# Kernel tuning notes

Hardware: AMD Instinct MI355X
Metric: run time of the kernel (lower is better)

## Reference

```python
import jax, jax.numpy as jnp
import numpy as np

N = 8192      # atoms
E = 4096      # edges (become transformer tokens)
E2 = 65536    # edges of second graph y
VOCAB = 119
DE = 200      # node_features == embedding_dim
D = 256
H = 8
L = 2
DFF = 2048


def _bn(x, g, b, eps=1e-6):
    m = x.mean(0)
    v = x.var(0)
    return (x - m) * jax.lax.rsqrt(v + eps) * g + b


def _ln(x, g, b, eps=1e-5):
    m = x.mean(-1, keepdims=True)
    v = ((x - m) ** 2).mean(-1, keepdims=True)
    return (x - m) * jax.lax.rsqrt(v + eps) * g + b


def _gcn(x, ei, W, b):
    # PyG GCNConv: add self loops, symmetric deg^-1/2 normalization
    n = x.shape[0]
    loop = jnp.arange(n)
    src = jnp.concatenate([ei[0], loop])
    dst = jnp.concatenate([ei[1], loop])
    deg = jax.ops.segment_sum(jnp.ones(src.shape[0], x.dtype), dst, num_segments=n)
    dinv = jnp.where(deg > 0, jax.lax.rsqrt(jnp.maximum(deg, 1e-12)), 0.0)
    msg = (x @ W)[src] * (dinv[src] * dinv[dst])[:, None]
    return jax.ops.segment_sum(msg, dst, num_segments=n) + b


def _mha(x, wi, bi, wo, bo):
    S, d = x.shape
    dh = d // H
    q, k, v = jnp.split(x @ wi + bi, 3, axis=1)
    q = q.reshape(S, H, dh)
    k = k.reshape(S, H, dh)
    v = v.reshape(S, H, dh)
    sc = jnp.einsum('qhd,khd->hqk', q, k) * (1.0 / np.sqrt(dh))
    a = jax.nn.softmax(sc, axis=-1)
    o = jnp.einsum('hqk,khd->qhd', a, v).reshape(S, d)
    return o @ wo + bo


def setup_inputs() -> dict:
    key = jax.random.key(0)
    ks = iter(jax.random.split(key, 64))
    nrm = lambda shape, s=0.05: jax.random.normal(next(ks), shape, jnp.float32) * s
    d = {}
    d['x'] = jax.random.randint(next(ks), (N,), 0, VOCAB)
    d['edge_index'] = jax.random.randint(next(ks), (2, E), 1, N + 1)  # 1-based, code subtracts 1
    d['pos'] = jax.random.normal(next(ks), (N, 3), jnp.float32)
    d['y'] = jax.random.randint(next(ks), (2, E2), 0, E)
    d['emb'] = nrm((VOCAB, DE), 1.0)
    d['fc1_w'] = nrm((1, DE))
    d['fc1_b'] = jnp.zeros((DE,), jnp.float32)
    d['bn4_g'] = jnp.ones((DE,), jnp.float32)
    d['bn4_b'] = jnp.zeros((DE,), jnp.float32)
    d['conv1_w'] = nrm((DE, D))
    d['conv1_b'] = jnp.zeros((D,), jnp.float32)
    d['conv2_w'] = nrm((D, D))
    d['conv2_b'] = jnp.zeros((D,), jnp.float32)
    for i in (1, 2, 3):
        d['bn%d_g' % i] = jnp.ones((D,), jnp.float32)
        d['bn%d_b' % i] = jnp.zeros((D,), jnp.float32)
    d['in_proj_w'] = nrm((L, D, 3 * D))
    d['in_proj_b'] = jnp.zeros((L, 3 * D), jnp.float32)
    d['out_proj_w'] = nrm((L, D, D))
    d['out_proj_b'] = jnp.zeros((L, D), jnp.float32)
    d['ln1_g'] = jnp.ones((L, D), jnp.float32)
    d['ln1_b'] = jnp.zeros((L, D), jnp.float32)
    d['ln2_g'] = jnp.ones((L, D), jnp.float32)
    d['ln2_b'] = jnp.zeros((L, D), jnp.float32)
    d['ff1_w'] = nrm((L, D, DFF))
    d['ff1_b'] = jnp.zeros((L, DFF), jnp.float32)
    d['ff2_w'] = nrm((L, DFF, D))
    d['ff2_b'] = jnp.zeros((L, D), jnp.float32)
    d['fc3_w'] = nrm((D, 1))
    d['fc3_b'] = jnp.zeros((1,), jnp.float32)
    d['fc4_w'] = nrm((D, 9))
    d['fc4_b'] = jnp.zeros((9,), jnp.float32)
    return d


def reference(x, edge_index, pos, y, emb, fc1_w, fc1_b, bn4_g, bn4_b,
              conv1_w, conv1_b, conv2_w, conv2_b,
              bn1_g, bn1_b, bn2_g, bn2_b, bn3_g, bn3_b,
              in_proj_w, in_proj_b, out_proj_w, out_proj_b,
              ln1_g, ln1_b, ln2_g, ln2_b, ff1_w, ff1_b, ff2_w, ff2_b,
              fc3_w, fc3_b, fc4_w, fc4_b):
    h = emb[x]                                   # [N, DE]
    ei = edge_index - 1
    row, col = ei[0], ei[1]
    ef = jnp.linalg.norm(pos[col] - pos[row], axis=1, keepdims=True)  # [E,1]
    ef = _bn(ef @ fc1_w + fc1_b, bn4_g, bn4_b)   # [E, DE]
    h = h[row] + h[col] + ef                     # [E, DE] edges -> tokens
    h = jax.nn.leaky_relu(_gcn(h, y, conv1_w, conv1_b))
    h = _bn(h, bn1_g, bn1_b)
    h = jax.nn.leaky_relu(h + _gcn(h, y, conv2_w, conv2_b))
    h = _bn(h, bn2_g, bn2_b)
    # post-norm TransformerEncoder (unbatched seq of length E), dropout=0
    for i in range(L):
        h = _ln(h + _mha(h, in_proj_w[i], in_proj_b[i], out_proj_w[i], out_proj_b[i]),
                ln1_g[i], ln1_b[i])
        ff = jax.nn.relu(h @ ff1_w[i] + ff1_b[i]) @ ff2_w[i] + ff2_b[i]
        h = _ln(h + ff, ln2_g[i], ln2_b[i])
    h = jax.nn.leaky_relu(h)
    h = _bn(h, bn3_g, bn3_b)
    sym_out = h @ fc3_w + fc3_b
    asym_out = h @ fc4_w + fc4_b
    return (sym_out, asym_out)
```

## Files before the change

### kernel.cpp

```cpp
#include <hip/hip_runtime.h>
#include <math.h>

#define ETOK 4096
#define NE2  65536
#define DEF  200
#define DM   256
#define NH   8
#define DH   32
#define DFFN 2048
#define NKS  4

#define QSCALE_LOG2E 0.25503474f

typedef __attribute__((ext_vector_type(8))) short bfrag8;
typedef __attribute__((ext_vector_type(4))) float f32x4;
typedef __attribute__((ext_vector_type(4))) short short4v;

__device__ __forceinline__ unsigned short f2bf(float f) {
  union { float f; unsigned u; } v; v.f = f;
  unsigned u = v.u + 0x7fffu + ((v.u >> 16) & 1u);
  return (unsigned short)(u >> 16);
}
__device__ __forceinline__ unsigned cvt_pk_bf16(float lo, float hi) {
  unsigned r;
  asm("v_cvt_pk_bf16_f32 %0, %1, %2" : "=v"(r) : "v"(lo), "v"(hi));
  return r;
}

__device__ __forceinline__ float wave_sum(float v) {
#pragma unroll
  for (int off = 32; off > 0; off >>= 1) v += __shfl_xor(v, off);
  return v;
}
__device__ __forceinline__ float block_sum(float v, float* red) {
  v = wave_sum(v);
  int lane = threadIdx.x & 63, w = threadIdx.x >> 6;
  if (lane == 0) red[w] = v;
  __syncthreads();
  float t = red[0] + red[1] + red[2] + red[3];
  __syncthreads();
  return t;
}

__global__ void edge_dist_kernel(const int* __restrict__ ei, const float* __restrict__ pos,
                                 float* __restrict__ ef0, float* __restrict__ stats) {
  __shared__ float red[4];
  int e = blockIdx.x * 256 + threadIdx.x;
  int r = ei[e] - 1;
  int c = ei[ETOK + e] - 1;
  float dx = pos[c * 3 + 0] - pos[r * 3 + 0];
  float dy = pos[c * 3 + 1] - pos[r * 3 + 1];
  float dz = pos[c * 3 + 2] - pos[r * 3 + 2];
  float d = sqrtf(dx * dx + dy * dy + dz * dz);
  ef0[e] = d;
  float s = block_sum(d, red);
  float s2 = block_sum(d * d, red);
  if (threadIdx.x == 0) {
    atomicAdd(stats + 0, s);
    atomicAdd(stats + 1, s2);
  }
}

__global__ void token_build_kernel(const int* __restrict__ x, const int* __restrict__ ei,
                                   const float* __restrict__ emb, const float* __restrict__ fc1_w,
                                   const float* __restrict__ bn4_g, const float* __restrict__ bn4_b,
                                   const float* __restrict__ ef0, const float* __restrict__ stats,
                                   unsigned short* __restrict__ tokbf) {
  int e = blockIdx.x;
  int j = threadIdx.x;
  float m = stats[0] * (1.0f / 4096.0f);
  float v = stats[1] * (1.0f / 4096.0f) - m * m;
  int xr = x[ei[e] - 1];
  int xc = x[ei[ETOK + e] - 1];
  float dd = ef0[e] - m;
  float val = 0.f;
  if (j < DEF) {
    float w = fc1_w[j];
    float s = w * rsqrtf(v * w * w + 1e-6f) * bn4_g[j];
    val = emb[(size_t)xr * DEF + j] + emb[(size_t)xc * DEF + j] + dd * s + bn4_b[j];
  }
  tokbf[(size_t)e * 256 + j] = f2bf(val);
}

__global__ void deg_count_kernel(const int* __restrict__ y, int* __restrict__ deg) {
  int e = blockIdx.x * 256 + threadIdx.x;
  atomicAdd(&deg[y[NE2 + e]], 1);
}
__global__ void dinv_kernel(const int* __restrict__ deg, float* __restrict__ dinv) {
  int i = blockIdx.x * 256 + threadIdx.x;
  dinv[i] = rsqrtf((float)(deg[i] + 1));
}
__global__ void scan_kernel(const int* __restrict__ deg, int* __restrict__ off,
                            int* __restrict__ cursor) {
  __shared__ int part[256];
  int t = threadIdx.x;
  int v[16];
  int s = 0;
#pragma unroll
  for (int i = 0; i < 16; ++i) {
    v[i] = deg[t * 16 + i];
    s += v[i];
  }
  part[t] = s;
  __syncthreads();
  if (t == 0) {
    int a = 0;
#pragma unroll 1
    for (int i = 0; i < 256; ++i) {
      int tmp = part[i];
      part[i] = a;
      a += tmp;
    }
    off[4096] = a;
  }
  __syncthreads();
  int a = part[t];
#pragma unroll
  for (int i = 0; i < 16; ++i) {
    off[t * 16 + i] = a;
    cursor[t * 16 + i] = a;
    a += v[i];
  }
}
__global__ void fill_kernel(const int* __restrict__ y, int* __restrict__ cursor,
                            int* __restrict__ srcl) {
  int e = blockIdx.x * 256 + threadIdx.x;
  int s = y[e];
  int d = y[NE2 + e];
  int slot = atomicAdd(&cursor[d], 1);
  srcl[slot] = s;
}

template <int RES, int ACT>
__global__ __launch_bounds__(256) void gather_kernel(const float* __restrict__ xw,
                                                     const int* __restrict__ off,
                                                     const int* __restrict__ srcl,
                                                     const float* __restrict__ dinv,
                                                     const float* __restrict__ bias,
                                                     const float* __restrict__ resid,
                                                     float* __restrict__ out) {
  __shared__ int slds[256];
  __shared__ float dlds[256];
  const int d = blockIdx.x;
  const int c = threadIdx.x;
  const int b0 = off[d], b1 = off[d + 1];
  const float dd = dinv[d];
  float acc = 0.f;
  for (int base = b0; base < b1; base += 256) {
    int n = min(256, b1 - base);
    __syncthreads();
    if (c < n) {
      int s = srcl[base + c];
      slds[c] = s;
      dlds[c] = dinv[s];
    }
    __syncthreads();
    for (int j = 0; j < n; ++j) {
      int s = slds[j];
      acc = fmaf(xw[(size_t)s * DM + c], dlds[j], acc);
    }
  }
  size_t idx = (size_t)d * DM + c;
  float v = bias[c] + xw[idx] * dd * dd + acc * dd;
  if (RES) v += resid[idx];
  if (ACT) v = v > 0.f ? v : 0.01f * v;
  out[idx] = v;
}

struct WEntry {
  const float* src;
  unsigned short* dst;
  int K, N, KP, tilesN, ntiles;
};
struct WPack {
  WEntry e[10];
};
__global__ __launch_bounds__(256) void wtrans_all_kernel(WPack p) {
  __shared__ float tl[32][33];
  int t = blockIdx.x;
  int i = 0;
  while (t >= p.e[i].ntiles) {
    t -= p.e[i].ntiles;
    ++i;
  }
  const WEntry w = p.e[i];
  int nb = (t % w.tilesN) * 32;
  int kb = (t / w.tilesN) * 32;
  int tx = threadIdx.x & 31, ty = threadIdx.x >> 5;
#pragma unroll
  for (int r = ty; r < 32; r += 8) {
    int k = kb + r, n = nb + tx;
    tl[r][tx] = (k < w.K && n < w.N) ? w.src[(size_t)k * w.N + n] : 0.f;
  }
  __syncthreads();
#pragma unroll
  for (int r = ty; r < 32; r += 8) {
    int n = nb + r, k = kb + tx;
    if (n < w.N) w.dst[(size_t)n * w.KP + k] = f2bf(tl[tx][r]);
  }
}

template <int BM, int BN, int OUTBF, int ACT, int QS>
__global__ __launch_bounds__(256) void mfma_gemm(const unsigned short* __restrict__ A,
                                                 const unsigned short* __restrict__ Bt,
                                                 const float* __restrict__ bias,
                                                 void* __restrict__ Cout, int M, int N, int K) {
  constexpr int BK = 64;
  constexpr int TM = BM / 32, TN = BN / 32;
  constexpr int ACH = BM / 32, BCH = BN / 32;
  __shared__ unsigned short Alds[BM * BK];
  __shared__ unsigned short Blds[BN * BK];
  const int tid = threadIdx.x;
  const int lane = tid & 63, wid = tid >> 6;
  const int g = lane >> 4, q = lane & 15;
  const int wr = wid >> 1, wc = wid & 1;
  const int m0 = blockIdx.y * BM, n0 = blockIdx.x * BN;

  f32x4 acc[TM][TN];
#pragma unroll
  for (int i = 0; i < TM; ++i)
#pragma unroll
    for (int j = 0; j < TN; ++j) acc[i][j] = (f32x4){0.f, 0.f, 0.f, 0.f};

  for (int k0 = 0; k0 < K; k0 += BK) {
    __syncthreads();
#pragma unroll
    for (int c = 0; c < ACH; ++c) {
      int chunk = wid * ACH + c;
      int row = chunk * 8 + (lane >> 3);
      int cb = ((lane & 7) * 16) ^ ((row & 7) << 4);
      const char* gp = (const char*)A + ((size_t)(m0 + row) * K + k0) * 2 + cb;
      __builtin_amdgcn_global_load_lds(
          (const __attribute__((address_space(1))) unsigned int*)gp,
          (__attribute__((address_space(3))) unsigned int*)(Alds + chunk * 512), 16, 0, 0);
    }
#pragma unroll
    for (int c = 0; c < BCH; ++c) {
      int chunk = wid * BCH + c;
      int row = chunk * 8 + (lane >> 3);
      int cb = ((lane & 7) * 16) ^ ((row & 7) << 4);
      const char* gp = (const char*)Bt + ((size_t)(n0 + row) * K + k0) * 2 + cb;
      __builtin_amdgcn_global_load_lds(
          (const __attribute__((address_space(1))) unsigned int*)gp,
          (__attribute__((address_space(3))) unsigned int*)(Blds + chunk * 512), 16, 0, 0);
    }
    __syncthreads();
#pragma unroll
    for (int ks = 0; ks < 2; ++ks) {
      bfrag8 af[TM], bfr[TN];
#pragma unroll
      for (int mi = 0; mi < TM; ++mi) {
        int row = wr * (BM / 2) + mi * 16 + q;
        int cb = (ks * 64 + g * 16) ^ ((row & 7) << 4);
        af[mi] = *(const bfrag8*)((const char*)Alds + row * 128 + cb);
      }
#pragma unroll
      for (int ni = 0; ni < TN; ++ni) {
        int row = wc * (BN / 2) + ni * 16 + q;
        int cb = (ks * 64 + g * 16) ^ ((row & 7) << 4);
        bfr[ni] = *(const bfrag8*)((const char*)Blds + row * 128 + cb);
      }
#pragma unroll
      for (int mi = 0; mi < TM; ++mi)
#pragma unroll
        for (int ni = 0; ni < TN; ++ni)
          acc[mi][ni] = __builtin_amdgcn_mfma_f32_16x16x32_bf16(af[mi], bfr[ni], acc[mi][ni], 0, 0, 0);
    }
  }
#pragma unroll
  for (int mi = 0; mi < TM; ++mi) {
    int row = m0 + wr * (BM / 2) + mi * 16 + g * 4;
#pragma unroll
    for (int ni = 0; ni < TN; ++ni) {
      int col = n0 + wc * (BN / 2) + ni * 16 + q;
      float bv = bias ? bias[col] : 0.f;
#pragma unroll
      for (int r = 0; r < 4; ++r) {
        float v = acc[mi][ni][r] + bv;
        if (QS && col < DM) v *= QSCALE_LOG2E;
        if (ACT == 1) v = fmaxf(v, 0.f);
        if (OUTBF)
          ((unsigned short*)Cout)[(size_t)(row + r) * N + col] = f2bf(v);
        else
          ((float*)Cout)[(size_t)(row + r) * N + col] = v;
      }
    }
  }
}

template <int LEAKY>
__global__ void col_stats_kernel(const float* __restrict__ x, int C, float* __restrict__ mean,
                                 float* __restrict__ var) {
  __shared__ float red[4];
  int c = blockIdx.x;
  float s = 0.f, s2 = 0.f;
  for (int r = threadIdx.x; r < ETOK; r += 256) {
    float v = x[(size_t)r * C + c];
    if (LEAKY) v = v > 0.f ? v : 0.01f * v;
    s += v;
    s2 += v * v;
  }
  float ts = block_sum(s, red);
  float ts2 = block_sum(s2, red);
  if (threadIdx.x == 0) {
    float m = ts * (1.0f / 4096.0f);
    mean[c] = m;
    var[c] = ts2 * (1.0f / 4096.0f) - m * m;
  }
}
template <int LEAKY>
__global__ void bn_apply_kernel(const float* __restrict__ x, const float* __restrict__ mean,
                                const float* __restrict__ var, const float* __restrict__ g,
                                const float* __restrict__ b, float* __restrict__ outf,
                                unsigned short* __restrict__ outb, int C) {
  size_t i = (size_t)blockIdx.x * 256 + threadIdx.x;
  int c = (int)(i % C);
  float v0 = x[i];
  if (LEAKY) v0 = v0 > 0.f ? v0 : 0.01f * v0;
  float v = (v0 - mean[c]) * rsqrtf(var[c] + 1e-6f) * g[c] + b[c];
  outf[i] = v;
  if (outb) outb[i] = f2bf(v);
}

__global__ __launch_bounds__(256) void attn_mfma_kernel(const unsigned short* __restrict__ qkv,
                                                        float* __restrict__ Opart,
                                                        float* __restrict__ MLpart) {
  const int h = blockIdx.y;
  const int qblk = blockIdx.x * 64;
  const int chunk = blockIdx.z;
  const int tid = threadIdx.x;
  const int wid = tid >> 6, lane = tid & 63;
  const int g = lane >> 4, q = lane & 15;

  __shared__ unsigned short Klds[64][40];
  __shared__ unsigned int Vtw[32][32];
  __shared__ unsigned short Plds[4][16][72];

  bfrag8 qfrag;
  {
    const unsigned short* qp = qkv + (size_t)(qblk + wid * 16 + q) * 768 + h * DH + g * 8;
    qfrag = *(const bfrag8*)qp;
  }
  const f32x4 zero = {0.f, 0.f, 0.f, 0.f};

  float m = -1e30f, lsum = 0.f;
  f32x4 o0 = zero, o1 = zero;

  const int kbeg = chunk * (ETOK / NKS);
  const int kend = kbeg + (ETOK / NKS);
  for (int kt = kbeg; kt < kend; kt += 64) {
    __syncthreads();
    {
      int key = tid >> 2, db = (tid & 3) * 8;
      const unsigned short* kp = qkv + (size_t)(kt + key) * 768 + DM + h * DH + db;
      *(bfrag8*)&Klds[key][db] = *(const bfrag8*)kp;

      int kp2 = tid >> 3, dc = (tid & 7) * 4;
      const unsigned short* v0 = qkv + (size_t)(kt + kp2 * 2) * 768 + 2 * DM + h * DH + dc;
      const unsigned short* v1 = v0 + 768;
      short4v a = *(const short4v*)v0;
      short4v bq = *(const short4v*)v1;
#pragma unroll
      for (int j = 0; j < 4; ++j) {
        int d = dc + j;
        unsigned pk = (unsigned)(unsigned short)a[j] | ((unsigned)(unsigned short)bq[j] << 16);
        Vtw[d][kp2 ^ (((d >> 3) & 3) << 3)] = pk;
      }
    }
    __syncthreads();

    f32x4 st[4];
    __builtin_amdgcn_s_setprio(1);
#pragma unroll
    for (int t = 0; t < 4; ++t) {
      bfrag8 kf = *(const bfrag8*)&Klds[t * 16 + q][g * 8];
      st[t] = __builtin_amdgcn_mfma_f32_16x16x32_bf16(kf, qfrag, zero, 0, 0, 0);
    }
    __builtin_amdgcn_s_setprio(0);

    float tmax = fmaxf(fmaxf(st[0][0], st[0][1]), fmaxf(st[0][2], st[0][3]));
#pragma unroll
    for (int t = 1; t < 4; ++t)
      tmax = fmaxf(tmax, fmaxf(fmaxf(st[t][0], st[t][1]), fmaxf(st[t][2], st[t][3])));
    tmax = fmaxf(tmax, __shfl_xor(tmax, 16));
    tmax = fmaxf(tmax, __shfl_xor(tmax, 32));
    if (!__all(tmax <= m + 8.0f)) {
      float mnew = fmaxf(m, tmax);
      float coef = __builtin_exp2f(m - mnew);
      lsum *= coef;
#pragma unroll
      for (int r = 0; r < 4; ++r) {
        float cr = __shfl(coef, g * 4 + r);
        o0[r] *= cr;
        o1[r] *= cr;
      }
      m = mnew;
    }

    float ps = 0.f;
    unsigned pk8[8];
#pragma unroll
    for (int t = 0; t < 4; ++t) {
      float p0 = __builtin_exp2f(st[t][0] - m);
      float p1 = __builtin_exp2f(st[t][1] - m);
      float p2 = __builtin_exp2f(st[t][2] - m);
      float p3 = __builtin_exp2f(st[t][3] - m);
      ps += (p0 + p1) + (p2 + p3);
      pk8[t * 2 + 0] = cvt_pk_bf16(p0, p1);
      pk8[t * 2 + 1] = cvt_pk_bf16(p2, p3);
    }
    lsum += ps;

#pragma unroll
    for (int t = 0; t < 4; ++t) {
      uint2 w2;
      w2.x = pk8[t * 2 + 0];
      w2.y = pk8[t * 2 + 1];
      *(uint2*)&Plds[wid][q][t * 16 + g * 4] = w2;
    }

    __builtin_amdgcn_s_setprio(1);
#pragma unroll
    for (int kg = 0; kg < 2; ++kg) {
      bfrag8 pa = *(const bfrag8*)&Plds[wid][q][kg * 32 + g * 8];
      int i0 = (kg * 16 + g * 4) ^ ((q >> 3) << 3);
      int i1 = (kg * 16 + g * 4) ^ (((2 + (q >> 3)) & 3) << 3);
      bfrag8 vb0 = *(const bfrag8*)&Vtw[q][i0];
      bfrag8 vb1 = *(const bfrag8*)&Vtw[16 + q][i1];
      o0 = __builtin_amdgcn_mfma_f32_16x16x32_bf16(pa, vb0, o0, 0, 0, 0);
      o1 = __builtin_amdgcn_mfma_f32_16x16x32_bf16(pa, vb1, o1, 0, 0, 0);
    }
    __builtin_amdgcn_s_setprio(0);
  }

  lsum += __shfl_xor(lsum, 16);
  lsum += __shfl_xor(lsum, 32);
#pragma unroll
  for (int r = 0; r < 4; ++r) {
    int row = qblk + wid * 16 + g * 4 + r;
    float* op = Opart + ((size_t)chunk * ETOK + row) * DM + h * DH;
    op[q] = o0[r];
    op[16 + q] = o1[r];
  }
  if (lane < 16) {
    int row = qblk + wid * 16 + lane;
    float* ml = MLpart + ((size_t)chunk * ETOK + row) * (NH * 2) + h * 2;
    ml[0] = m;
    ml[1] = lsum;
  }
}

__global__ __launch_bounds__(256) void attn_combine_kernel(const float* __restrict__ Opart,
                                                           const float* __restrict__ MLpart,
                                                           unsigned short* __restrict__ out) {
  __shared__ float mls[NKS][NH][2];
  const int row = blockIdx.x;
  const int c = threadIdx.x;
  if (c < NKS * NH * 2) {
    int ch = c >> 4, rem = c & 15;
    mls[ch][rem >> 1][rem & 1] = MLpart[((size_t)ch * ETOK + row) * (NH * 2) + rem];
  }
  __syncthreads();
  const int h = c >> 5;
  float mstar = mls[0][h][0];
#pragma unroll
  for (int ch = 1; ch < NKS; ++ch) mstar = fmaxf(mstar, mls[ch][h][0]);
  float lstar = 0.f, acc = 0.f;
#pragma unroll
  for (int ch = 0; ch < NKS; ++ch) {
    float w = __builtin_exp2f(mls[ch][h][0] - mstar);
    lstar = fmaf(mls[ch][h][1], w, lstar);
    acc = fmaf(Opart[((size_t)ch * ETOK + row) * DM + c], w, acc);
  }
  out[(size_t)row * DM + c] = f2bf(acc / lstar);
}

__global__ void add_ln_kernel(const float* __restrict__ x, const float* __restrict__ r,
                              float* __restrict__ outf, unsigned short* __restrict__ outb,
                              const float* __restrict__ g, const float* __restrict__ b) {
  __shared__ float red[4];
  int row = blockIdx.x, t = threadIdx.x;
  size_t idx = (size_t)row * DM + t;
  float v = x[idx] + r[idx];
  float mean = block_sum(v, red) * (1.0f / 256.0f);
  float dv = v - mean;
  float var = block_sum(dv * dv, red) * (1.0f / 256.0f);
  float o = dv * rsqrtf(var + 1e-5f) * g[t] + b[t];
  outf[idx] = o;
  outb[idx] = f2bf(o);
}

__global__ void head_kernel(const float* __restrict__ h, const float* __restrict__ fc3w,
                            const float* __restrict__ fc3b, const float* __restrict__ fc4w,
                            const float* __restrict__ fc4b, float* __restrict__ out) {
  int wave = threadIdx.x >> 6, lane = threadIdx.x & 63;
  int tok = blockIdx.x * 4 + wave;
  const float* hr = h + (size_t)tok * DM;
  float hv[4];
#pragma unroll
  for (int i = 0; i < 4; ++i) hv[i] = hr[lane * 4 + i];
  float acc = 0.f;
#pragma unroll
  for (int i = 0; i < 4; ++i) acc += hv[i] * fc3w[lane * 4 + i];
  acc = wave_sum(acc);
  if (lane == 0) out[tok] = acc + fc3b[0];
#pragma unroll
  for (int j = 0; j < 9; ++j) {
    float a = 0.f;
#pragma unroll
    for (int i = 0; i < 4; ++i) a += hv[i] * fc4w[(lane * 4 + i) * 9 + j];
    a = wave_sum(a);
    if (lane == 0) out[ETOK + (size_t)tok * 9 + j] = a + fc4b[j];
  }
}

extern "C" void kernel_launch(void* const* d_in, const int* in_sizes, int n_in,
                              void* d_out, int out_size, void* d_ws, size_t ws_size,
                              hipStream_t stream) {
  const int* x = (const int*)d_in[0];
  const int* edge_index = (const int*)d_in[1];
  const float* pos = (const float*)d_in[2];
  const int* y = (const int*)d_in[3];
  const float* emb = (const float*)d_in[4];
  const float* fc1_w = (const float*)d_in[5];
  const float* bn4_g = (const float*)d_in[7];
  const float* bn4_b = (const float*)d_in[8];
  const float* conv1_w = (const float*)d_in[9];
  const float* conv1_b = (const float*)d_in[10];
  const float* conv2_w = (const float*)d_in[11];
  const float* conv2_b = (const float*)d_in[12];
  const float* bn1_g = (const float*)d_in[13];
  const float* bn1_b = (const float*)d_in[14];
  const float* bn2_g = (const float*)d_in[15];
  const float* bn2_b = (const float*)d_in[16];
  const float* bn3_g = (const float*)d_in[17];
  const float* bn3_b = (const float*)d_in[18];
  const float* ipw = (const float*)d_in[19];
  const float* ipb = (const float*)d_in[20];
  const float* opw = (const float*)d_in[21];
  const float* opb = (const float*)d_in[22];
  const float* ln1_g = (const float*)d_in[23];
  const float* ln1_b = (const float*)d_in[24];
  const float* ln2_g = (const float*)d_in[25];
  const float* ln2_b = (const float*)d_in[26];
  const float* ff1w = (const float*)d_in[27];
  const float* ff1b = (const float*)d_in[28];
  const float* ff2w = (const float*)d_in[29];
  const float* ff2b = (const float*)d_in[30];
  const float* fc3w = (const float*)d_in[31];
  const float* fc3b = (const float*)d_in[32];
  const float* fc4w = (const float*)d_in[33];
  const float* fc4b = (const float*)d_in[34];
  float* outp = (float*)d_out;

  char* wsp = (char*)d_ws;
  auto alloc = [&](size_t bytes) {
    void* p = (void*)wsp;
    wsp += (bytes + 255) & ~(size_t)255;
    return p;
  };
  unsigned short* big_bf = (unsigned short*)alloc((size_t)ETOK * DFFN * 2);
  unsigned short* attno = (unsigned short*)alloc((size_t)ETOK * DM * 2);
  unsigned short* h_bf = (unsigned short*)alloc((size_t)ETOK * DM * 2);
  unsigned short* tok_bf = (unsigned short*)alloc((size_t)ETOK * 256 * 2);
  float* hf = (float*)alloc((size_t)ETOK * DM * 4);
  float* t1 = (float*)alloc((size_t)ETOK * DM * 4);
  float* t2 = (float*)alloc((size_t)ETOK * DM * 4);
  float* Opart = (float*)alloc((size_t)NKS * ETOK * DM * 4);
  float* MLpart = (float*)alloc((size_t)NKS * ETOK * NH * 2 * 4);
  unsigned short* c1wt = (unsigned short*)alloc(256 * 256 * 2);
  unsigned short* c2wt = (unsigned short*)alloc(256 * 256 * 2);
  unsigned short* ipwt = (unsigned short*)alloc((size_t)2 * 768 * 256 * 2);
  unsigned short* opwt = (unsigned short*)alloc((size_t)2 * 256 * 256 * 2);
  unsigned short* f1wt = (unsigned short*)alloc((size_t)2 * 2048 * 256 * 2);
  unsigned short* f2wt = (unsigned short*)alloc((size_t)2 * 256 * 2048 * 2);
  float* ef0 = (float*)alloc(ETOK * 4);
  float* dinv = (float*)alloc(ETOK * 4);
  int* deg = (int*)alloc(ETOK * 4);
  int* off = (int*)alloc((ETOK + 1) * 4);
  int* cursor = (int*)alloc(ETOK * 4);
  int* srcl = (int*)alloc(NE2 * 4);
  float* stats = (float*)alloc(8 * 4);
  float* colm = (float*)alloc(DM * 4);
  float* colv = (float*)alloc(DM * 4);

  hipMemsetAsync(stats, 0, 2 * sizeof(float), stream);
  hipMemsetAsync(deg, 0, ETOK * sizeof(int), stream);

  WPack wp;
  int ntot = 0;
  auto went = [&](int i, const float* src, unsigned short* dst, int K, int N, int KP) {
    wp.e[i].src = src;
    wp.e[i].dst = dst;
    wp.e[i].K = K;
    wp.e[i].N = N;
    wp.e[i].KP = KP;
    wp.e[i].tilesN = (N + 31) / 32;
    wp.e[i].ntiles = ((N + 31) / 32) * (KP / 32);
    ntot += wp.e[i].ntiles;
  };
  went(0, conv1_w, c1wt, 200, 256, 256);
  went(1, conv2_w, c2wt, 256, 256, 256);
  went(2, ipw, ipwt, 256, 768, 256);
  went(3, ipw + (size_t)256 * 768, ipwt + (size_t)768 * 256, 256, 768, 256);
  went(4, opw, opwt, 256, 256, 256);
  went(5, opw + (size_t)256 * 256, opwt + (size_t)256 * 256, 256, 256, 256);
  went(6, ff1w, f1wt, 256, 2048, 256);
  went(7, ff1w + (size_t)256 * 2048, f1wt + (size_t)2048 * 256, 256, 2048, 256);
  went(8, ff2w, f2wt, 2048, 256, 2048);
  went(9, ff2w + (size_t)2048 * 256, f2wt + (size_t)256 * 2048, 2048, 256, 2048);
  wtrans_all_kernel<<<ntot, 256, 0, stream>>>(wp);

  edge_dist_kernel<<<16, 256, 0, stream>>>(edge_index, pos, ef0, stats);
  deg_count_kernel<<<NE2 / 256, 256, 0, stream>>>(y, deg);
  scan_kernel<<<1, 256, 0, stream>>>(deg, off, cursor);
  dinv_kernel<<<ETOK / 256, 256, 0, stream>>>(deg, dinv);
  fill_kernel<<<NE2 / 256, 256, 0, stream>>>(y, cursor, srcl);
  token_build_kernel<<<ETOK, 256, 0, stream>>>(x, edge_index, emb, fc1_w, bn4_g, bn4_b, ef0,
                                               stats, tok_bf);

  mfma_gemm<32, 32, 0, 0, 0><<<dim3(8, 128), 256, 0, stream>>>(tok_bf, c1wt, nullptr, t1, ETOK, DM, 256);
  gather_kernel<0, 1><<<ETOK, 256, 0, stream>>>(t1, off, srcl, dinv, conv1_b, nullptr, t2);
  col_stats_kernel<0><<<DM, 256, 0, stream>>>(t2, DM, colm, colv);
  bn_apply_kernel<0><<<ETOK * DM / 256, 256, 0, stream>>>(t2, colm, colv, bn1_g, bn1_b, hf, h_bf, DM);

  mfma_gemm<32, 32, 0, 0, 0><<<dim3(8, 128), 256, 0, stream>>>(h_bf, c2wt, nullptr, t1, ETOK, DM, 256);
  gather_kernel<1, 1><<<ETOK, 256, 0, stream>>>(t1, off, srcl, dinv, conv2_b, hf, t2);
  col_stats_kernel<0><<<DM, 256, 0, stream>>>(t2, DM, colm, colv);
  bn_apply_kernel<0><<<ETOK * DM / 256, 256, 0, stream>>>(t2, colm, colv, bn2_g, bn2_b, hf, h_bf, DM);

  for (int i = 0; i < 2; ++i) {
    mfma_gemm<32, 32, 1, 0, 1><<<dim3(24, 128), 256, 0, stream>>>(
        h_bf, ipwt + (size_t)i * 768 * 256, ipb + (size_t)i * 768, big_bf, ETOK, 768, 256);
    attn_mfma_kernel<<<dim3(ETOK / 64, NH, NKS), 256, 0, stream>>>(big_bf, Opart, MLpart);
    attn_combine_kernel<<<ETOK, 256, 0, stream>>>(Opart, MLpart, attno);
    mfma_gemm<32, 32, 0, 0, 0><<<dim3(8, 128), 256, 0, stream>>>(
        attno, opwt + (size_t)i * 256 * 256, opb + (size_t)i * DM, t2, ETOK, DM, 256);
    add_ln_kernel<<<ETOK, 256, 0, stream>>>(t2, hf, hf, h_bf, ln1_g + (size_t)i * DM,
                                            ln1_b + (size_t)i * DM);
    mfma_gemm<64, 64, 1, 1, 0><<<dim3(32, 64), 256, 0, stream>>>(
        h_bf, f1wt + (size_t)i * 2048 * 256, ff1b + (size_t)i * DFFN, big_bf, ETOK, DFFN, 256);
    mfma_gemm<32, 32, 0, 0, 0><<<dim3(8, 128), 256, 0, stream>>>(
        big_bf, f2wt + (size_t)i * 256 * 2048, ff2b + (size_t)i * DM, t2, ETOK, DM, 2048);
    add_ln_kernel<<<ETOK, 256, 0, stream>>>(t2, hf, hf, h_bf, ln2_g + (size_t)i * DM,
                                            ln2_b + (size_t)i * DM);
  }

  col_stats_kernel<1><<<DM, 256, 0, stream>>>(hf, DM, colm, colv);
  bn_apply_kernel<1><<<ETOK * DM / 256, 256, 0, stream>>>(hf, colm, colv, bn3_g, bn3_b, hf, nullptr, DM);
  head_kernel<<<ETOK / 4, 256, 0, stream>>>(hf, fc3w, fc3b, fc4w, fc4b, outp);
}
```

Before: 373.3 us.

## Double-buffer attention K/V staging, store partials in bf16, coalesce BN column stats

Attention now prefetches the next K/V tile into registers while computing on a double-buffered LDS tile, dropping one barrier per iteration. Partial attention outputs are stored as bf16 instead of fp32, halving that write and read traffic at some precision cost. The BatchNorm column-statistics kernel is replaced by a coalesced row-block accumulator using atomics, with mean and variance computed in the apply kernel. The dinv computation is folded into the scan kernel to remove one launch.

```diff
diff --git a/kernel.cpp b/kernel.cpp
--- a/kernel.cpp
+++ b/kernel.cpp
@@ -20,6 +20,11 @@
   union { float f; unsigned u; } v; v.f = f;
   unsigned u = v.u + 0x7fffu + ((v.u >> 16) & 1u);
   return (unsigned short)(u >> 16);
+}
+__device__ __forceinline__ float bf2f(unsigned short u) {
+  union { unsigned u; float f; } v;
+  v.u = ((unsigned)u) << 16;
+  return v.f;
 }
 __device__ __forceinline__ unsigned cvt_pk_bf16(float lo, float hi) {
   unsigned r;
@@ -86,12 +91,8 @@
   int e = blockIdx.x * 256 + threadIdx.x;
   atomicAdd(&deg[y[NE2 + e]], 1);
 }
-__global__ void dinv_kernel(const int* __restrict__ deg, float* __restrict__ dinv) {
-  int i = blockIdx.x * 256 + threadIdx.x;
-  dinv[i] = rsqrtf((float)(deg[i] + 1));
-}
 __global__ void scan_kernel(const int* __restrict__ deg, int* __restrict__ off,
-                            int* __restrict__ cursor) {
+                            int* __restrict__ cursor, float* __restrict__ dinv) {
   __shared__ int part[256];
   int t = threadIdx.x;
   int v[16];
@@ -119,6 +120,7 @@
   for (int i = 0; i < 16; ++i) {
     off[t * 16 + i] = a;
     cursor[t * 16 + i] = a;
+    dinv[t * 16 + i] = rsqrtf((float)(v[i] + 1));
     a += v[i];
   }
 }
@@ -289,41 +291,40 @@
 }
 
 template <int LEAKY>
-__global__ void col_stats_kernel(const float* __restrict__ x, int C, float* __restrict__ mean,
-                                 float* __restrict__ var) {
-  __shared__ float red[4];
-  int c = blockIdx.x;
+__global__ __launch_bounds__(256) void col_accum_kernel(const float* __restrict__ x,
+                                                        float* __restrict__ colm,
+                                                        float* __restrict__ colv) {
+  int c = threadIdx.x;
+  int r0 = blockIdx.x * 16;
   float s = 0.f, s2 = 0.f;
-  for (int r = threadIdx.x; r < ETOK; r += 256) {
-    float v = x[(size_t)r * C + c];
+#pragma unroll
+  for (int i = 0; i < 16; ++i) {
+    float v = x[(size_t)(r0 + i) * DM + c];
     if (LEAKY) v = v > 0.f ? v : 0.01f * v;
     s += v;
     s2 += v * v;
   }
-  float ts = block_sum(s, red);
-  float ts2 = block_sum(s2, red);
-  if (threadIdx.x == 0) {
-    float m = ts * (1.0f / 4096.0f);
-    mean[c] = m;
-    var[c] = ts2 * (1.0f / 4096.0f) - m * m;
-  }
+  atomicAdd(&colm[c], s);
+  atomicAdd(&colv[c], s2);
 }
 template <int LEAKY>
-__global__ void bn_apply_kernel(const float* __restrict__ x, const float* __restrict__ mean,
-                                const float* __restrict__ var, const float* __restrict__ g,
+__global__ void bn_apply_kernel(const float* __restrict__ x, const float* __restrict__ colm,
+                                const float* __restrict__ colv, const float* __restrict__ g,
                                 const float* __restrict__ b, float* __restrict__ outf,
                                 unsigned short* __restrict__ outb, int C) {
   size_t i = (size_t)blockIdx.x * 256 + threadIdx.x;
   int c = (int)(i % C);
+  float mean = colm[c] * (1.0f / 4096.0f);
+  float var = colv[c] * (1.0f / 4096.0f) - mean * mean;
   float v0 = x[i];
   if (LEAKY) v0 = v0 > 0.f ? v0 : 0.01f * v0;
-  float v = (v0 - mean[c]) * rsqrtf(var[c] + 1e-6f) * g[c] + b[c];
+  float v = (v0 - mean) * rsqrtf(var + 1e-6f) * g[c] + b[c];
   outf[i] = v;
   if (outb) outb[i] = f2bf(v);
 }
 
 __global__ __launch_bounds__(256) void attn_mfma_kernel(const unsigned short* __restrict__ qkv,
-                                                        float* __restrict__ Opart,
+                                                        unsigned short* __restrict__ Opart,
                                                         float* __restrict__ MLpart) {
   const int h = blockIdx.y;
   const int qblk = blockIdx.x * 64;
@@ -332,8 +333,8 @@
   const int wid = tid >> 6, lane = tid & 63;
   const int g = lane >> 4, q = lane & 15;
 
-  __shared__ unsigned short Klds[64][40];
-  __shared__ unsigned int Vtw[32][32];
+  __shared__ unsigned short Klds[2][64][40];
+  __shared__ unsigned int Vtw[2][32][32];
   __shared__ unsigned short Plds[4][16][72];
 
   bfrag8 qfrag;
@@ -343,45 +344,57 @@
   }
   const f32x4 zero = {0.f, 0.f, 0.f, 0.f};
 
+  const int skey = tid >> 2;
+  const int sdb = (tid & 3) * 8;
+  const int kp2 = tid >> 3;
+  const int dc = (tid & 7) * 4;
+
+  const int kbeg = chunk * (ETOK / NKS);
+  const int NT = (ETOK / NKS) / 64;
+
+  const unsigned short* kptr = qkv + (size_t)(kbeg + skey) * 768 + DM + h * DH + sdb;
+  const unsigned short* vptr = qkv + (size_t)(kbeg + kp2 * 2) * 768 + 2 * DM + h * DH + dc;
+
+  bfrag8 kreg = *(const bfrag8*)kptr;
+  kptr += 64 * 768;
+  short4v va = *(const short4v*)vptr;
+  short4v vb = *(const short4v*)(vptr + 768);
+  vptr += 64 * 768;
+
   float m = -1e30f, lsum = 0.f;
   f32x4 o0 = zero, o1 = zero;
 
-  const int kbeg = chunk * (ETOK / NKS);
-  const int kend = kbeg + (ETOK / NKS);
-  for (int kt = kbeg; kt < kend; kt += 64) {
+  for (int t = 0; t < NT; ++t) {
+    const int buf = t & 1;
+    *(bfrag8*)&Klds[buf][skey][sdb] = kreg;
+#pragma unroll
+    for (int j = 0; j < 4; ++j) {
+      int d = dc + j;
+      unsigned pkv = (unsigned)(unsigned short)va[j] | ((unsigned)(unsigned short)vb[j] << 16);
+      Vtw[buf][d][kp2 ^ (((d >> 3) & 3) << 3)] = pkv;
+    }
     __syncthreads();
-    {
-      int key = tid >> 2, db = (tid & 3) * 8;
-      const unsigned short* kp = qkv + (size_t)(kt + key) * 768 + DM + h * DH + db;
-      *(bfrag8*)&Klds[key][db] = *(const bfrag8*)kp;
-
-      int kp2 = tid >> 3, dc = (tid & 7) * 4;
-      const unsigned short* v0 = qkv + (size_t)(kt + kp2 * 2) * 768 + 2 * DM + h * DH + dc;
-      const unsigned short* v1 = v0 + 768;
-      short4v a = *(const short4v*)v0;
-      short4v bq = *(const short4v*)v1;
-#pragma unroll
-      for (int j = 0; j < 4; ++j) {
-        int d = dc + j;
-        unsigned pk = (unsigned)(unsigned short)a[j] | ((unsigned)(unsigned short)bq[j] << 16);
-        Vtw[d][kp2 ^ (((d >> 3) & 3) << 3)] = pk;
-      }
-    }
-    __syncthreads();
+    if (t + 1 < NT) {
+      kreg = *(const bfrag8*)kptr;
+      kptr += 64 * 768;
+      va = *(const short4v*)vptr;
+      vb = *(const short4v*)(vptr + 768);
+      vptr += 64 * 768;
+    }
 
     f32x4 st[4];
     __builtin_amdgcn_s_setprio(1);
 #pragma unroll
-    for (int t = 0; t < 4; ++t) {
-      bfrag8 kf = *(const bfrag8*)&Klds[t * 16 + q][g * 8];
-      st[t] = __builtin_amdgcn_mfma_f32_16x16x32_bf16(kf, qfrag, zero, 0, 0, 0);
+    for (int tt = 0; tt < 4; ++tt) {
+      bfrag8 kf = *(const bfrag8*)&Klds[buf][tt * 16 + q][g * 8];
+      st[tt] = __builtin_amdgcn_mfma_f32_16x16x32_bf16(kf, qfrag, zero, 0, 0, 0);
     }
     __builtin_amdgcn_s_setprio(0);
 
     float tmax = fmaxf(fmaxf(st[0][0], st[0][1]), fmaxf(st[0][2], st[0][3]));
 #pragma unroll
-    for (int t = 1; t < 4; ++t)
-      tmax = fmaxf(tmax, fmaxf(fmaxf(st[t][0], st[t][1]), fmaxf(st[t][2], st[t][3])));
+    for (int tt = 1; tt < 4; ++tt)
+      tmax = fmaxf(tmax, fmaxf(fmaxf(st[tt][0], st[tt][1]), fmaxf(st[tt][2], st[tt][3])));
     tmax = fmaxf(tmax, __shfl_xor(tmax, 16));
     tmax = fmaxf(tmax, __shfl_xor(tmax, 32));
     if (!__all(tmax <= m + 8.0f)) {
@@ -400,23 +413,23 @@
     float ps = 0.f;
     unsigned pk8[8];
 #pragma unroll
-    for (int t = 0; t < 4; ++t) {
-      float p0 = __builtin_exp2f(st[t][0] - m);
-      float p1 = __builtin_exp2f(st[t][1] - m);
-      float p2 = __builtin_exp2f(st[t][2] - m);
-      float p3 = __builtin_exp2f(st[t][3] - m);
+    for (int tt = 0; tt < 4; ++tt) {
+      float p0 = __builtin_exp2f(st[tt][0] - m);
+      float p1 = __builtin_exp2f(st[tt][1] - m);
+      float p2 = __builtin_exp2f(st[tt][2] - m);
+      float p3 = __builtin_exp2f(st[tt][3] - m);
       ps += (p0 + p1) + (p2 + p3);
-      pk8[t * 2 + 0] = cvt_pk_bf16(p0, p1);
-      pk8[t * 2 + 1] = cvt_pk_bf16(p2, p3);
+      pk8[tt * 2 + 0] = cvt_pk_bf16(p0, p1);
+      pk8[tt * 2 + 1] = cvt_pk_bf16(p2, p3);
     }
     lsum += ps;
 
 #pragma unroll
-    for (int t = 0; t < 4; ++t) {
+    for (int tt = 0; tt < 4; ++tt) {
       uint2 w2;
-      w2.x = pk8[t * 2 + 0];
-      w2.y = pk8[t * 2 + 1];
-      *(uint2*)&Plds[wid][q][t * 16 + g * 4] = w2;
+      w2.x = pk8[tt * 2 + 0];
+      w2.y = pk8[tt * 2 + 1];
+      *(uint2*)&Plds[wid][q][tt * 16 + g * 4] = w2;
     }
 
     __builtin_amdgcn_s_setprio(1);
@@ -425,8 +438,8 @@
       bfrag8 pa = *(const bfrag8*)&Plds[wid][q][kg * 32 + g * 8];
       int i0 = (kg * 16 + g * 4) ^ ((q >> 3) << 3);
       int i1 = (kg * 16 + g * 4) ^ (((2 + (q >> 3)) & 3) << 3);
-      bfrag8 vb0 = *(const bfrag8*)&Vtw[q][i0];
-      bfrag8 vb1 = *(const bfrag8*)&Vtw[16 + q][i1];
+      bfrag8 vb0 = *(const bfrag8*)&Vtw[buf][q][i0];
+      bfrag8 vb1 = *(const bfrag8*)&Vtw[buf][16 + q][i1];
       o0 = __builtin_amdgcn_mfma_f32_16x16x32_bf16(pa, vb0, o0, 0, 0, 0);
       o1 = __builtin_amdgcn_mfma_f32_16x16x32_bf16(pa, vb1, o1, 0, 0, 0);
     }
@@ -438,9 +451,9 @@
 #pragma unroll
   for (int r = 0; r < 4; ++r) {
     int row = qblk + wid * 16 + g * 4 + r;
-    float* op = Opart + ((size_t)chunk * ETOK + row) * DM + h * DH;
-    op[q] = o0[r];
-    op[16 + q] = o1[r];
+    unsigned short* op = Opart + ((size_t)chunk * ETOK + row) * DM + h * DH;
+    op[q] = f2bf(o0[r]);
+    op[16 + q] = f2bf(o1[r]);
   }
   if (lane < 16) {
     int row = qblk + wid * 16 + lane;
@@ -450,7 +463,7 @@
   }
 }
 
-__global__ __launch_bounds__(256) void attn_combine_kernel(const float* __restrict__ Opart,
+__global__ __launch_bounds__(256) void attn_combine_kernel(const unsigned short* __restrict__ Opart,
                                                            const float* __restrict__ MLpart,
                                                            unsigned short* __restrict__ out) {
   __shared__ float mls[NKS][NH][2];
@@ -470,7 +483,7 @@
   for (int ch = 0; ch < NKS; ++ch) {
     float w = __builtin_exp2f(mls[ch][h][0] - mstar);
     lstar = fmaf(mls[ch][h][1], w, lstar);
-    acc = fmaf(Opart[((size_t)ch * ETOK + row) * DM + c], w, acc);
+    acc = fmaf(bf2f(Opart[((size_t)ch * ETOK + row) * DM + c]), w, acc);
   }
   out[(size_t)row * DM + c] = f2bf(acc / lstar);
 }
@@ -566,7 +579,7 @@
   float* hf = (float*)alloc((size_t)ETOK * DM * 4);
   float* t1 = (float*)alloc((size_t)ETOK * DM * 4);
   float* t2 = (float*)alloc((size_t)ETOK * DM * 4);
-  float* Opart = (float*)alloc((size_t)NKS * ETOK * DM * 4);
+  unsigned short* Opart = (unsigned short*)alloc((size_t)NKS * ETOK * DM * 2);
   float* MLpart = (float*)alloc((size_t)NKS * ETOK * NH * 2 * 4);
   unsigned short* c1wt = (unsigned short*)alloc(256 * 256 * 2);
   unsigned short* c2wt = (unsigned short*)alloc(256 * 256 * 2);
@@ -613,20 +626,23 @@
 
   edge_dist_kernel<<<16, 256, 0, stream>>>(edge_index, pos, ef0, stats);
   deg_count_kernel<<<NE2 / 256, 256, 0, stream>>>(y, deg);
-  scan_kernel<<<1, 256, 0, stream>>>(deg, off, cursor);
-  dinv_kernel<<<ETOK / 256, 256, 0, stream>>>(deg, dinv);
+  scan_kernel<<<1, 256, 0, stream>>>(deg, off, cursor, dinv);
   fill_kernel<<<NE2 / 256, 256, 0, stream>>>(y, cursor, srcl);
   token_build_kernel<<<ETOK, 256, 0, stream>>>(x, edge_index, emb, fc1_w, bn4_g, bn4_b, ef0,
                                                stats, tok_bf);
 
   mfma_gemm<32, 32, 0, 0, 0><<<dim3(8, 128), 256, 0, stream>>>(tok_bf, c1wt, nullptr, t1, ETOK, DM, 256);
   gather_kernel<0, 1><<<ETOK, 256, 0, stream>>>(t1, off, srcl, dinv, conv1_b, nullptr, t2);
-  col_stats_kernel<0><<<DM, 256, 0, stream>>>(t2, DM, colm, colv);
+  hipMemsetAsync(colm, 0, DM * sizeof(float), stream);
+  hipMemsetAsync(colv, 0, DM * sizeof(float), stream);
+  col_accum_kernel<0><<<ETOK / 16, 256, 0, stream>>>(t2, colm, colv);
   bn_apply_kernel<0><<<ETOK * DM / 256, 256, 0, stream>>>(t2, colm, colv, bn1_g, bn1_b, hf, h_bf, DM);
 
   mfma_gemm<32, 32, 0, 0, 0><<<dim3(8, 128), 256, 0, stream>>>(h_bf, c2wt, nullptr, t1, ETOK, DM, 256);
   gather_kernel<1, 1><<<ETOK, 256, 0, stream>>>(t1, off, srcl, dinv, conv2_b, hf, t2);
-  col_stats_kernel<0><<<DM, 256, 0, stream>>>(t2, DM, colm, colv);
+  hipMemsetAsync(colm, 0, DM * sizeof(float), stream);
+  hipMemsetAsync(colv, 0, DM * sizeof(float), stream);
+  col_accum_kernel<0><<<ETOK / 16, 256, 0, stream>>>(t2, colm, colv);
   bn_apply_kernel<0><<<ETOK * DM / 256, 256, 0, stream>>>(t2, colm, colv, bn2_g, bn2_b, hf, h_bf, DM);
 
   for (int i = 0; i < 2; ++i) {
@@ -646,7 +662,9 @@
                                             ln2_b + (size_t)i * DM);
   }
 
-  col_stats_kernel<1><<<DM, 256, 0, stream>>>(hf, DM, colm, colv);
+  hipMemsetAsync(colm, 0, DM * sizeof(float), stream);
+  hipMemsetAsync(colv, 0, DM * sizeof(float), stream);
+  col_accum_kernel<1><<<ETOK / 16, 256, 0, stream>>>(hf, colm, colv);
   bn_apply_kernel<1><<<ETOK * DM / 256, 256, 0, stream>>>(hf, colm, colv, bn3_g, bn3_b, hf, nullptr, DM);
   head_kernel<<<ETOK / 4, 256, 0, stream>>>(hf, fc3w, fc3b, fc4w, fc4b, outp);
 }
```

Result: no change. 371.8 us (-0.4%).
